# Performance work log

Measured on AMD Instinct MI355X. Metric: run time of the kernel, lower is better.

The kernel has to match this reference:

```python
import jax, jax.numpy as jnp
import numpy as np

N_NODES = 100000
N_EDGES = 1600000
IN_CH, HID_CH, OUT_CH, NCLASS = 128, 256, 256, 40


def gcn_conv(x, edge_index, edge_weight, W, b):
    """PyG GCNConv: h = D^{-1/2} (A + I) D^{-1/2} (x @ W) + b, weighted edges."""
    n = x.shape[0]
    row, col = edge_index[0], edge_index[1]
    loop = jnp.arange(n)
    row = jnp.concatenate([row, loop])
    col = jnp.concatenate([col, loop])
    ew = jnp.concatenate([edge_weight, jnp.ones((n,), x.dtype)])  # self-loop weight 1
    deg = jax.ops.segment_sum(ew, col, num_segments=n)
    dinv = jnp.where(deg > 0, jax.lax.rsqrt(deg), 0.0)
    norm = dinv[row] * ew * dinv[col]            # [E+N]
    h = x @ W                                    # transform before propagate (as PyG)
    msg = h[row] * norm[:, None]                 # gather + scale, [E+N, F]
    out = jax.ops.segment_sum(msg, col, num_segments=n)  # scatter-add
    return out + b


def setup_inputs() -> dict:
    key = jax.random.key(0)
    ks = jax.random.split(key, 9)
    x = jax.random.normal(ks[0], (N_NODES, IN_CH), dtype=jnp.float32)
    edge_index = jax.random.randint(ks[1], (2, N_EDGES), 0, N_NODES, dtype=jnp.int64)
    edge_attr = jax.random.uniform(ks[2], (N_EDGES,), dtype=jnp.float32)
    s1 = 1.0 / np.sqrt(IN_CH)
    s2 = 1.0 / np.sqrt(HID_CH)
    s3 = 1.0 / np.sqrt(OUT_CH)
    W1 = jax.random.uniform(ks[3], (IN_CH, HID_CH), jnp.float32, -s1, s1)
    b1 = jnp.zeros((HID_CH,), jnp.float32)
    W2 = jax.random.uniform(ks[4], (HID_CH, OUT_CH), jnp.float32, -s2, s2)
    b2 = jnp.zeros((OUT_CH,), jnp.float32)
    fcW = jax.random.uniform(ks[5], (OUT_CH, NCLASS), jnp.float32, -s3, s3)
    fcb = jax.random.uniform(ks[6], (NCLASS,), jnp.float32, -s3, s3)
    return {"x": x, "edge_index": edge_index, "edge_attr": edge_attr,
            "W1": W1, "b1": b1, "W2": W2, "b2": b2, "fcW": fcW, "fcb": fcb}


def reference(x, edge_index, edge_attr, W1, b1, W2, b2, fcW, fcb):
    # eval mode: dropout is identity
    h = jax.nn.relu(gcn_conv(x, edge_index, edge_attr, W1, b1))
    h = jax.nn.relu(gcn_conv(h, edge_index, edge_attr, W2, b2))
    return h @ fcW + fcb
```

## Files before the change

kernel.cpp:

```cpp
#include <hip/hip_runtime.h>

#define NODES 100000
#define EDGES 1600000

typedef __attribute__((ext_vector_type(4))) float floatx4;
typedef _Float16 h16;
typedef __attribute__((ext_vector_type(4))) _Float16 h16x4;
typedef __attribute__((ext_vector_type(8))) _Float16 h16x8;
typedef __attribute__((ext_vector_type(8))) _Float16 half8;

#define WSCALE 64.0f
#define WINV   (1.0f / 64.0f)

__device__ inline void load_lds16(void* lds, const void* g) {
    __builtin_amdgcn_global_load_lds((const __attribute__((address_space(1))) void*)g,
                                     (__attribute__((address_space(3))) void*)lds, 16, 0, 0);
}

__device__ inline float meta_w(unsigned m) {
    return (float)__builtin_bit_cast(h16, (unsigned short)(m & 0x7FFFu));
}

__global__ __launch_bounds__(256) void k_init(unsigned long long* __restrict__ packed, int n) {
    int i = blockIdx.x * 256 + threadIdx.x;
    if (i < n) packed[i] = 0ull;
}

__device__ inline void w_split(const float* W, h16* Wh, h16* Wl, int idx, int K) {
    int k = idx >> 8, nn = idx & 255;
    float v = W[idx] * WSCALE;
    h16 h = (h16)v;
    h16 l = (h16)(v - (float)h);
    Wh[nn * K + k] = h;
    Wl[nn * K + k] = l;
}

__global__ __launch_bounds__(256) void k_hist(unsigned long long* __restrict__ packed,
                                              unsigned short* __restrict__ rank,
                                              const int* __restrict__ col,
                                              const float* __restrict__ ew, int e,
                                              const float* __restrict__ W1, h16* __restrict__ W1h, h16* __restrict__ W1l,
                                              const float* __restrict__ W2, h16* __restrict__ W2h, h16* __restrict__ W2l,
                                              const float* __restrict__ x, h16* __restrict__ x16, int n) {
    int b = blockIdx.x;
    if (b < 6250) {
        int i = b * 256 + threadIdx.x;
        if (i < e) {
            int c = col[i];
            unsigned long long v = (1ull << 40) |
                (unsigned long long)__float2uint_rn(ew[i] * 1048576.0f);
            unsigned long long old = atomicAdd(&packed[c], v);
            rank[i] = (unsigned short)(old >> 40);
        }
    } else if (b < 6378) {
        w_split(W1, W1h, W1l, (b - 6250) * 256 + threadIdx.x, 128);
    } else if (b < 6634) {
        w_split(W2, W2h, W2l, (b - 6378) * 256 + threadIdx.x, 256);
    } else {
        int i = (b - 6634) * 256 + threadIdx.x;
        if (i < n * 32) {
            float4 v = reinterpret_cast<const float4*>(x)[i];
            h16x4 h;
            h.x = (h16)v.x; h.y = (h16)v.y; h.z = (h16)v.z; h.w = (h16)v.w;
            reinterpret_cast<h16x4*>(x16)[i] = h;
        }
    }
}

__global__ __launch_bounds__(256) void k_scan1(const unsigned long long* __restrict__ packed,
                                               int* __restrict__ rowptr,
                                               int* __restrict__ partials,
                                               float* __restrict__ dinv, int n) {
    __shared__ int wtot[4];
    const int tid = threadIdx.x, lane = tid & 63, wid = tid >> 6;
    int i = blockIdx.x * 256 + tid;
    int v = 0;
    if (i < n) {
        unsigned long long p = packed[i];
        v = (int)(p >> 40);
        float deg = 1.0f + (float)(p & 0xFFFFFFFFFFull) * (1.0f / 1048576.0f);
        dinv[i] = rsqrtf(deg);
    }
    int incl = v;
#pragma unroll
    for (int off = 1; off < 64; off <<= 1) {
        int t = __shfl_up(incl, off, 64);
        if (lane >= off) incl += t;
    }
    if (lane == 63) wtot[wid] = incl;
    __syncthreads();
    int woff = 0;
    for (int k = 0; k < wid; ++k) woff += wtot[k];
    if (i < n) rowptr[i] = woff + incl - v;
    if (tid == 255) partials[blockIdx.x] = woff + incl;
}

__global__ __launch_bounds__(512) void k_scan2(int* __restrict__ partials, int nb) {
    __shared__ int wtot[8];
    const int tid = threadIdx.x, lane = tid & 63, wid = tid >> 6;
    int v = (tid < nb) ? partials[tid] : 0;
    int incl = v;
#pragma unroll
    for (int off = 1; off < 64; off <<= 1) {
        int t = __shfl_up(incl, off, 64);
        if (lane >= off) incl += t;
    }
    if (lane == 63) wtot[wid] = incl;
    __syncthreads();
    int woff = 0;
    for (int k = 0; k < wid; ++k) woff += wtot[k];
    if (tid < nb) partials[tid] = woff + incl - v;
}

__global__ __launch_bounds__(256) void k_scan3(int* __restrict__ rowptr,
                                               const int* __restrict__ partials, int n) {
    int i = blockIdx.x * 256 + threadIdx.x;
    if (i < n) rowptr[i] += partials[blockIdx.x];
    if (blockIdx.x == 0 && threadIdx.x == 0) rowptr[n] = EDGES;
}

__global__ __launch_bounds__(256) void k_build(const int* __restrict__ rowptr,
                                               const unsigned short* __restrict__ rank,
                                               unsigned* __restrict__ meta,
                                               const int* __restrict__ row, const int* __restrict__ col,
                                               const float* __restrict__ ew,
                                               const float* __restrict__ dinv, int e) {
    int i = blockIdx.x * 256 + threadIdx.x;
    if (i >= e) return;
    int r = row[i], c = col[i];
    float w = dinv[r] * ew[i] * dinv[c];
    unsigned short wb = __builtin_bit_cast(unsigned short, (h16)w);
    meta[rowptr[c] + rank[i]] = ((unsigned)r << 15) | wb;
}

__global__ __launch_bounds__(256) void k_gather_x(h16* __restrict__ Xa,
                                                  const h16* __restrict__ x16,
                                                  const float* __restrict__ dinv,
                                                  const int* __restrict__ rowptr,
                                                  const unsigned* __restrict__ meta, int n) {
    int node = (blockIdx.x << 2) + (threadIdx.x >> 6);
    if (node >= n) return;
    const int lane = threadIdx.x & 63;
    const int half = lane >> 5;
    const int cb = (lane & 31) << 2;
    float a0[4] = {}, a1[4] = {};
    int p = rowptr[node];
    const int end = rowptr[node + 1];
    for (; p + 3 < end; p += 4) {
        unsigned m0 = meta[p + half], m1 = meta[p + half + 2];
        h16x4 h0 = *(const h16x4*)(x16 + (size_t)(m0 >> 15) * 128 + cb);
        h16x4 h1 = *(const h16x4*)(x16 + (size_t)(m1 >> 15) * 128 + cb);
        float w0 = meta_w(m0), w1 = meta_w(m1);
#pragma unroll
        for (int j = 0; j < 4; ++j) {
            a0[j] = fmaf((float)h0[j], w0, a0[j]);
            a1[j] = fmaf((float)h1[j], w1, a1[j]);
        }
    }
    for (; p + 1 < end; p += 2) {
        unsigned m0 = meta[p + half];
        h16x4 h0 = *(const h16x4*)(x16 + (size_t)(m0 >> 15) * 128 + cb);
        float w0 = meta_w(m0);
#pragma unroll
        for (int j = 0; j < 4; ++j) a0[j] = fmaf((float)h0[j], w0, a0[j]);
    }
    if (half == 0 && p < end) {
        unsigned m0 = meta[p];
        h16x4 h0 = *(const h16x4*)(x16 + (size_t)(m0 >> 15) * 128 + cb);
        float w0 = meta_w(m0);
#pragma unroll
        for (int j = 0; j < 4; ++j) a1[j] = fmaf((float)h0[j], w0, a1[j]);
    }
#pragma unroll
    for (int j = 0; j < 4; ++j) a0[j] += a1[j];
#pragma unroll
    for (int j = 0; j < 4; ++j) a0[j] += __shfl(a0[j], lane + 32);
    if (half == 0) {
        float s = dinv[node]; s = s * s;
        h16x4 sv = *(const h16x4*)(x16 + (size_t)node * 128 + cb);
        h16x4 o;
#pragma unroll
        for (int j = 0; j < 4; ++j) o[j] = (h16)fmaf((float)sv[j], s, a0[j]);
        *(h16x4*)(Xa + (size_t)node * 128 + cb) = o;
    }
}

__global__ __launch_bounds__(256) void k_gather_y(h16* __restrict__ Y,
                                                  const h16* __restrict__ P1,
                                                  const float* __restrict__ dinv,
                                                  const int* __restrict__ rowptr,
                                                  const unsigned* __restrict__ meta, int n) {
    int node = (blockIdx.x << 2) + (threadIdx.x >> 6);
    if (node >= n) return;
    const int lane = threadIdx.x & 63;
    const int half = lane >> 5;
    const int cb = (lane & 31) << 3;
    float a0[8] = {}, a1[8] = {};
    int p = rowptr[node];
    const int end = rowptr[node + 1];
    for (; p + 3 < end; p += 4) {
        unsigned m0 = meta[p + half], m1 = meta[p + half + 2];
        h16x8 h0 = *(const h16x8*)(P1 + (size_t)(m0 >> 15) * 256 + cb);
        h16x8 h1 = *(const h16x8*)(P1 + (size_t)(m1 >> 15) * 256 + cb);
        float w0 = meta_w(m0), w1 = meta_w(m1);
#pragma unroll
        for (int j = 0; j < 8; ++j) {
            a0[j] = fmaf((float)h0[j], w0, a0[j]);
            a1[j] = fmaf((float)h1[j], w1, a1[j]);
        }
    }
    for (; p + 1 < end; p += 2) {
        unsigned m0 = meta[p + half];
        h16x8 h0 = *(const h16x8*)(P1 + (size_t)(m0 >> 15) * 256 + cb);
        float w0 = meta_w(m0);
#pragma unroll
        for (int j = 0; j < 8; ++j) a0[j] = fmaf((float)h0[j], w0, a0[j]);
    }
    if (half == 0 && p < end) {
        unsigned m0 = meta[p];
        h16x8 h0 = *(const h16x8*)(P1 + (size_t)(m0 >> 15) * 256 + cb);
        float w0 = meta_w(m0);
#pragma unroll
        for (int j = 0; j < 8; ++j) a1[j] = fmaf((float)h0[j], w0, a1[j]);
    }
#pragma unroll
    for (int j = 0; j < 8; ++j) a0[j] += a1[j];
#pragma unroll
    for (int j = 0; j < 8; ++j) a0[j] += __shfl(a0[j], lane + 32);
    if (half == 0) {
        float s = dinv[node]; s = s * s;
        h16x8 sv = *(const h16x8*)(P1 + (size_t)node * 256 + cb);
        h16x8 o;
#pragma unroll
        for (int j = 0; j < 8; ++j) o[j] = (h16)fmaf((float)sv[j], s, a0[j]);
        *(h16x8*)(Y + (size_t)node * 256 + cb) = o;
    }
}

__global__ __launch_bounds__(256) void k_gemm1(const h16* __restrict__ Ag,
                                               const h16* __restrict__ Bhg,
                                               const h16* __restrict__ Blg,
                                               h16* __restrict__ Out,
                                               const float* __restrict__ bias,
                                               int M, int K) {
    __shared__ __attribute__((aligned(16))) char ldsA[8192];
    __shared__ __attribute__((aligned(16))) char ldsBh[8192];
    __shared__ __attribute__((aligned(16))) char ldsBl[8192];
    const int tid = threadIdx.x;
    const int lane = tid & 63, wid = tid >> 6;
    const int quad = lane >> 4, l16 = lane & 15;
    const int rowBase = blockIdx.x * 128;
    const int colBase = blockIdx.y * 128;
    const int wm = (wid & 1) * 64, wn = (wid >> 1) * 64;

    floatx4 acc[4][4] = {};

    const int c0 = wid * 64 + lane;
    const int c1 = c0 + 256;
    const int r0 = ((c0 >> 6) << 4) + (c0 & 15), q0 = (c0 >> 4) & 3;
    const int r1 = ((c1 >> 6) << 4) + (c1 & 15), q1 = (c1 >> 4) & 3;
    const size_t aoff0 = (size_t)(rowBase + r0) * K + q0 * 8;
    const size_t aoff1 = (size_t)(rowBase + r1) * K + q1 * 8;
    const size_t boff0 = (size_t)(colBase + r0) * K + q0 * 8;
    const size_t boff1 = (size_t)(colBase + r1) * K + q1 * 8;
    const int lo0 = (wid * 64) * 16;
    const int lo1 = (256 + wid * 64) * 16;

    for (int k0 = 0; k0 < K; k0 += 32) {
        load_lds16(ldsA + lo0, Ag + aoff0 + k0);
        load_lds16(ldsA + lo1, Ag + aoff1 + k0);
        load_lds16(ldsBh + lo0, Bhg + boff0 + k0);
        load_lds16(ldsBh + lo1, Bhg + boff1 + k0);
        load_lds16(ldsBl + lo0, Blg + boff0 + k0);
        load_lds16(ldsBl + lo1, Blg + boff1 + k0);
        __syncthreads();

        const half8* vA  = (const half8*)ldsA;
        const half8* vBh = (const half8*)ldsBh;
        const half8* vBl = (const half8*)ldsBl;
        half8 af[4], bfh[4], bfl[4];
#pragma unroll
        for (int mi = 0; mi < 4; ++mi)
            af[mi] = vA[((wm >> 4) + mi) * 64 + quad * 16 + l16];
#pragma unroll
        for (int ni = 0; ni < 4; ++ni) {
            int idx = ((wn >> 4) + ni) * 64 + quad * 16 + l16;
            bfh[ni] = vBh[idx];
            bfl[ni] = vBl[idx];
        }
#pragma unroll
        for (int mi = 0; mi < 4; ++mi)
#pragma unroll
            for (int ni = 0; ni < 4; ++ni) {
                acc[mi][ni] = __builtin_amdgcn_mfma_f32_16x16x32_f16(af[mi], bfh[ni], acc[mi][ni], 0, 0, 0);
                acc[mi][ni] = __builtin_amdgcn_mfma_f32_16x16x32_f16(af[mi], bfl[ni], acc[mi][ni], 0, 0, 0);
            }
        __syncthreads();
    }

#pragma unroll
    for (int mi = 0; mi < 4; ++mi) {
#pragma unroll
        for (int r = 0; r < 4; ++r) {
            int grow = rowBase + wm + mi * 16 + quad * 4 + r;
            if (grow < M) {
#pragma unroll
                for (int ni = 0; ni < 4; ++ni) {
                    int gcol = colBase + wn + ni * 16 + l16;
                    float v = fmaxf(acc[mi][ni][r] * WINV + bias[gcol], 0.f);
                    Out[(size_t)grow * 256 + gcol] = (h16)v;
                }
            }
        }
    }
}

__global__ __launch_bounds__(256, 2) void k_gemm2fc(const h16* __restrict__ Y,
                                                    const h16* __restrict__ Bhg,
                                                    const h16* __restrict__ Blg,
                                                    const float* __restrict__ b2,
                                                    const float* __restrict__ fcW,
                                                    const float* __restrict__ fcb,
                                                    float* __restrict__ out, int M) {
    __shared__ __attribute__((aligned(16))) char lds[67584];
    char* ldsA  = lds;
    char* ldsBh = lds + 8192;
    char* ldsBl = lds + 24576;
    const int tid = threadIdx.x;
    const int lane = tid & 63, wid = tid >> 6;
    const int quad = lane >> 4, l16 = lane & 15;
    const int rowBase = blockIdx.x * 128;
    const int wm = (wid & 1) * 64, wn = (wid >> 1) * 128;

    floatx4 acc[4][8] = {};

    for (int k0 = 0; k0 < 256; k0 += 32) {
#pragma unroll
        for (int i = 0; i < 2; ++i) {
            int c = tid + i * 256;
            int r = ((c >> 6) << 4) + (c & 15), q = (c >> 4) & 3;
            load_lds16(ldsA + c * 16, Y + (size_t)(rowBase + r) * 256 + k0 + q * 8);
        }
#pragma unroll
        for (int i = 0; i < 4; ++i) {
            int c = tid + i * 256;
            int r = ((c >> 6) << 4) + (c & 15), q = (c >> 4) & 3;
            size_t go = (size_t)r * 256 + k0 + q * 8;
            load_lds16(ldsBh + c * 16, Bhg + go);
            load_lds16(ldsBl + c * 16, Blg + go);
        }
        __syncthreads();

        const half8* vA  = (const half8*)ldsA;
        const half8* vBh = (const half8*)ldsBh;
        const half8* vBl = (const half8*)ldsBl;
        half8 af[4];
#pragma unroll
        for (int mi = 0; mi < 4; ++mi)
            af[mi] = vA[((wm >> 4) + mi) * 64 + quad * 16 + l16];
#pragma unroll
        for (int ni = 0; ni < 8; ++ni) {
            int bidx = ((wn >> 4) + ni) * 64 + quad * 16 + l16;
            half8 bh = vBh[bidx];
            half8 bl = vBl[bidx];
#pragma unroll
            for (int mi = 0; mi < 4; ++mi) {
                acc[mi][ni] = __builtin_amdgcn_mfma_f32_16x16x32_f16(af[mi], bh, acc[mi][ni], 0, 0, 0);
                acc[mi][ni] = __builtin_amdgcn_mfma_f32_16x16x32_f16(af[mi], bl, acc[mi][ni], 0, 0, 0);
            }
        }
        __syncthreads();
    }

    h16* P2s = (h16*)lds;
#pragma unroll
    for (int mi = 0; mi < 4; ++mi)
#pragma unroll
        for (int r = 0; r < 4; ++r) {
            int lrow = wm + mi * 16 + quad * 4 + r;
#pragma unroll
            for (int ni = 0; ni < 8; ++ni) {
                int col = wn + ni * 16 + l16;
                float v = fmaxf(acc[mi][ni][r] * WINV + b2[col], 0.f);
                P2s[lrow * 264 + col] = (h16)v;
            }
        }
    __syncthreads();

    const int myrow = (wid & 1) * 64 + lane;
    const int jb = (wid >> 1) * 20;
    const int grow = rowBase + myrow;
    float fa[20] = {};
    for (int kc = 0; kc < 32; ++kc) {
        h16x8 xv8 = *(const h16x8*)(P2s + myrow * 264 + kc * 8);
        float xv[8];
#pragma unroll
        for (int j = 0; j < 8; ++j) xv[j] = (float)xv8[j];
#pragma unroll
        for (int kk = 0; kk < 8; ++kk) {
            const float* wrow = fcW + (kc * 8 + kk) * 40 + jb;
#pragma unroll
            for (int j = 0; j < 20; ++j)
                fa[j] = fmaf(xv[kk], wrow[j], fa[j]);
        }
    }
    if (grow < M) {
#pragma unroll
        for (int j = 0; j < 20; ++j)
            out[(size_t)grow * 40 + jb + j] = fa[j] + fcb[jb + j];
    }
}

extern "C" void kernel_launch(void* const* d_in, const int* in_sizes, int n_in,
                              void* d_out, int out_size, void* d_ws, size_t ws_size,
                              hipStream_t stream) {
    const float* x   = (const float*)d_in[0];
    const int*   ei  = (const int*)d_in[1];
    const float* ea  = (const float*)d_in[2];
    const float* W1  = (const float*)d_in[3];
    const float* b1  = (const float*)d_in[4];
    const float* W2  = (const float*)d_in[5];
    const float* b2  = (const float*)d_in[6];
    const float* fcW = (const float*)d_in[7];
    const float* fcb = (const float*)d_in[8];
    float* out = (float*)d_out;

    const int n = NODES, e = EDGES;
    const int* row = ei;
    const int* col = ei + e;

    char* ws = (char*)d_ws;
    char*  Areg   = ws;
    char*  Breg   = ws + 102400000u;
    float* dinv   = (float*)(ws + 204800000u);
    unsigned long long* packed = (unsigned long long*)(ws + 205200000u);
    int*   rowptr = (int*)  (ws + 206000000u);
    unsigned* meta = (unsigned*)(ws + 206400016u);
    h16*   W1h    = (h16*)  (ws + 212800016u);
    h16*   W1l    = (h16*)  (ws + 212865552u);
    h16*   W2h    = (h16*)  (ws + 212931088u);
    h16*   W2l    = (h16*)  (ws + 213062160u);

    int* partials = (int*)Areg;
    h16* Xa16 = (h16*)Areg;
    h16* x16  = (h16*)(Areg + 25600000u);
    h16* Yh   = (h16*)Areg;
    unsigned short* rank = (unsigned short*)Breg;
    h16* P1   = (h16*)Breg;

    const int nb = (n + 255) / 256;
    const int eb = e / 256;

    k_init<<<nb, 256, 0, stream>>>(packed, n);
    k_hist<<<19134, 256, 0, stream>>>(packed, rank, col, ea, e,
                                      W1, W1h, W1l, W2, W2h, W2l, x, x16, n);
    k_scan1<<<nb, 256, 0, stream>>>(packed, rowptr, partials, dinv, n);
    k_scan2<<<1, 512, 0, stream>>>(partials, nb);
    k_scan3<<<nb, 256, 0, stream>>>(rowptr, partials, n);
    k_build<<<eb, 256, 0, stream>>>(rowptr, rank, meta, row, col, ea, dinv, e);

    k_gather_x<<<(n + 3) / 4, 256, 0, stream>>>(Xa16, x16, dinv, rowptr, meta, n);
    dim3 gg((n + 127) / 128, 2);
    k_gemm1<<<gg, 256, 0, stream>>>(Xa16, W1h, W1l, P1, b1, n, 128);

    k_gather_y<<<(n + 3) / 4, 256, 0, stream>>>(Yh, P1, dinv, rowptr, meta, n);
    k_gemm2fc<<<(n + 127) / 128, 256, 0, stream>>>(Yh, W2h, W2l, b2, fcW, fcb, out, n);
}
```

Before: 664.5 us.

## Split fused GEMM2+FC kernel into generic GEMM and separate FC kernel

The fused second-layer GEMM plus final linear kernel is replaced by two launches: the generic split-fp16 MFMA GEMM (now reused for layer 2 with a 2-column-block grid) writes a half-precision intermediate to workspace, then a new scalar FC kernel stages fcW and transposed activations in LDS to compute the 40-class output. The aim is to drop the fused kernel's large LDS footprint and register pressure (limited occupancy, serial FC tail). In exchange it adds an extra 51 MB round trip through global memory for the intermediate and one more launch.

```diff
diff --git a/kernel.cpp b/kernel.cpp
--- a/kernel.cpp
+++ b/kernel.cpp
@@ -237,12 +237,12 @@
     }
 }
 
-__global__ __launch_bounds__(256) void k_gemm1(const h16* __restrict__ Ag,
-                                               const h16* __restrict__ Bhg,
-                                               const h16* __restrict__ Blg,
-                                               h16* __restrict__ Out,
-                                               const float* __restrict__ bias,
-                                               int M, int K) {
+__global__ __launch_bounds__(256) void k_gemm(const h16* __restrict__ Ag,
+                                              const h16* __restrict__ Bhg,
+                                              const h16* __restrict__ Blg,
+                                              h16* __restrict__ Out,
+                                              const float* __restrict__ bias,
+                                              int M, int K) {
     __shared__ __attribute__((aligned(16))) char ldsA[8192];
     __shared__ __attribute__((aligned(16))) char ldsBh[8192];
     __shared__ __attribute__((aligned(16))) char ldsBl[8192];
@@ -315,99 +315,45 @@
     }
 }
 
-__global__ __launch_bounds__(256, 2) void k_gemm2fc(const h16* __restrict__ Y,
-                                                    const h16* __restrict__ Bhg,
-                                                    const h16* __restrict__ Blg,
-                                                    const float* __restrict__ b2,
-                                                    const float* __restrict__ fcW,
-                                                    const float* __restrict__ fcb,
-                                                    float* __restrict__ out, int M) {
-    __shared__ __attribute__((aligned(16))) char lds[67584];
-    char* ldsA  = lds;
-    char* ldsBh = lds + 8192;
-    char* ldsBl = lds + 24576;
+__global__ __launch_bounds__(256) void k_fc(float* __restrict__ out, const h16* __restrict__ X,
+                                            const float* __restrict__ W, const float* __restrict__ bias,
+                                            int M) {
+    __shared__ float Ws[256 * 40];
+    __shared__ float Xs[32][69];
     const int tid = threadIdx.x;
-    const int lane = tid & 63, wid = tid >> 6;
-    const int quad = lane >> 4, l16 = lane & 15;
-    const int rowBase = blockIdx.x * 128;
-    const int wm = (wid & 1) * 64, wn = (wid >> 1) * 128;
-
-    floatx4 acc[4][8] = {};
+#pragma unroll
+    for (int t = 0; t < 10; ++t) {
+        int idx = (t * 256 + tid) * 4;
+        *reinterpret_cast<float4*>(&Ws[idx]) = *reinterpret_cast<const float4*>(W + idx);
+    }
+    const int rowBase = blockIdx.x * 64;
+    const int r  = tid >> 2;
+    const int cg = (tid & 3) * 10;
+    const int kq = (tid & 3) << 3;
+    float acc[10] = {};
 
     for (int k0 = 0; k0 < 256; k0 += 32) {
-#pragma unroll
-        for (int i = 0; i < 2; ++i) {
-            int c = tid + i * 256;
-            int r = ((c >> 6) << 4) + (c & 15), q = (c >> 4) & 3;
-            load_lds16(ldsA + c * 16, Y + (size_t)(rowBase + r) * 256 + k0 + q * 8);
-        }
-#pragma unroll
-        for (int i = 0; i < 4; ++i) {
-            int c = tid + i * 256;
-            int r = ((c >> 6) << 4) + (c & 15), q = (c >> 4) & 3;
-            size_t go = (size_t)r * 256 + k0 + q * 8;
-            load_lds16(ldsBh + c * 16, Bhg + go);
-            load_lds16(ldsBl + c * 16, Blg + go);
-        }
+        int rr = rowBase + r;
+        h16x8 v = {};
+        if (rr < M) v = *reinterpret_cast<const h16x8*>(X + (size_t)rr * 256 + k0 + kq);
+#pragma unroll
+        for (int j = 0; j < 8; ++j) Xs[kq + j][r] = (float)v[j];
         __syncthreads();
-
-        const half8* vA  = (const half8*)ldsA;
-        const half8* vBh = (const half8*)ldsBh;
-        const half8* vBl = (const half8*)ldsBl;
-        half8 af[4];
-#pragma unroll
-        for (int mi = 0; mi < 4; ++mi)
-            af[mi] = vA[((wm >> 4) + mi) * 64 + quad * 16 + l16];
-#pragma unroll
-        for (int ni = 0; ni < 8; ++ni) {
-            int bidx = ((wn >> 4) + ni) * 64 + quad * 16 + l16;
-            half8 bh = vBh[bidx];
-            half8 bl = vBl[bidx];
-#pragma unroll
-            for (int mi = 0; mi < 4; ++mi) {
-                acc[mi][ni] = __builtin_amdgcn_mfma_f32_16x16x32_f16(af[mi], bh, acc[mi][ni], 0, 0, 0);
-                acc[mi][ni] = __builtin_amdgcn_mfma_f32_16x16x32_f16(af[mi], bl, acc[mi][ni], 0, 0, 0);
-            }
+#pragma unroll
+        for (int kk = 0; kk < 32; ++kk) {
+            float xv = Xs[kk][r];
+#pragma unroll
+            for (int j = 0; j < 10; ++j)
+                acc[j] = fmaf(xv, Ws[(k0 + kk) * 40 + cg + j], acc[j]);
         }
         __syncthreads();
     }
 
-    h16* P2s = (h16*)lds;
-#pragma unroll
-    for (int mi = 0; mi < 4; ++mi)
-#pragma unroll
-        for (int r = 0; r < 4; ++r) {
-            int lrow = wm + mi * 16 + quad * 4 + r;
-#pragma unroll
-            for (int ni = 0; ni < 8; ++ni) {
-                int col = wn + ni * 16 + l16;
-                float v = fmaxf(acc[mi][ni][r] * WINV + b2[col], 0.f);
-                P2s[lrow * 264 + col] = (h16)v;
-            }
-        }
-    __syncthreads();
-
-    const int myrow = (wid & 1) * 64 + lane;
-    const int jb = (wid >> 1) * 20;
-    const int grow = rowBase + myrow;
-    float fa[20] = {};
-    for (int kc = 0; kc < 32; ++kc) {
-        h16x8 xv8 = *(const h16x8*)(P2s + myrow * 264 + kc * 8);
-        float xv[8];
-#pragma unroll
-        for (int j = 0; j < 8; ++j) xv[j] = (float)xv8[j];
-#pragma unroll
-        for (int kk = 0; kk < 8; ++kk) {
-            const float* wrow = fcW + (kc * 8 + kk) * 40 + jb;
-#pragma unroll
-            for (int j = 0; j < 20; ++j)
-                fa[j] = fmaf(xv[kk], wrow[j], fa[j]);
-        }
-    }
-    if (grow < M) {
-#pragma unroll
-        for (int j = 0; j < 20; ++j)
-            out[(size_t)grow * 40 + jb + j] = fa[j] + fcb[jb + j];
+    int orow = rowBase + r;
+    if (orow < M) {
+#pragma unroll
+        for (int j = 0; j < 10; ++j)
+            out[(size_t)orow * 40 + cg + j] = acc[j] + bias[cg + j];
     }
 }
 
@@ -447,6 +393,7 @@
     h16* Yh   = (h16*)Areg;
     unsigned short* rank = (unsigned short*)Breg;
     h16* P1   = (h16*)Breg;
+    h16* P2h  = (h16*)(Breg + 51200000u);
 
     const int nb = (n + 255) / 256;
     const int eb = e / 256;
@@ -459,10 +406,13 @@
     k_scan3<<<nb, 256, 0, stream>>>(rowptr, partials, n);
     k_build<<<eb, 256, 0, stream>>>(rowptr, rank, meta, row, col, ea, dinv, e);
 
+    dim3 gg((n + 127) / 128, 2);
+
     k_gather_x<<<(n + 3) / 4, 256, 0, stream>>>(Xa16, x16, dinv, rowptr, meta, n);
-    dim3 gg((n + 127) / 128, 2);
-    k_gemm1<<<gg, 256, 0, stream>>>(Xa16, W1h, W1l, P1, b1, n, 128);
+    k_gemm<<<gg, 256, 0, stream>>>(Xa16, W1h, W1l, P1, b1, n, 128);
 
     k_gather_y<<<(n + 3) / 4, 256, 0, stream>>>(Yh, P1, dinv, rowptr, meta, n);
-    k_gemm2fc<<<(n + 127) / 128, 256, 0, stream>>>(Yh, W2h, W2l, b2, fcW, fcb, out, n);
-}
+    k_gemm<<<gg, 256, 0, stream>>>(Yh, W2h, W2l, P2h, b2, n, 256);
+
+    k_fc<<<(n + 63) / 64, 256, 0, stream>>>(out, P2h, fcW, fcb, n);
+}
```

Result: faster. 612.2 us (-7.9%).
